# Kernel optimization log

Measured on AMD Instinct MI355X. Metric: run time of the kernel, lower is better.

Reference implementation:

```python
import jax, jax.numpy as jnp
import numpy as np

N_WORDS = 30000
EMB_DIM = 784  # 28*28
MAT_DIM = 28
BATCH = 1024
SEQ_LEN = 64


def setup_inputs() -> dict:
    key = jax.random.key(0)
    k_sent, k_tab = jax.random.split(key)
    # token ids in [0, n_words]; row 0 is the neutral (identity) / padding element
    sent = jax.random.randint(k_sent, (BATCH, SEQ_LEN), 0, N_WORDS + 1, dtype=jnp.int32).astype(jnp.int64)
    eye_flat = jnp.eye(MAT_DIM, dtype=jnp.float32).reshape(-1)
    # 'identity' init strategy: identity + small gaussian noise (scale kept small for stability of long products)
    table = eye_flat + 0.01 * jax.random.normal(k_tab, (N_WORDS + 1, EMB_DIM), dtype=jnp.float32)
    table = table.at[0].set(eye_flat)  # neutral element at padding_idx=0
    return {"sent": sent, "table": table}


def reference(sent, table):
    # sent: [B, S] int ids; table: [n_words+1, d*d]
    B, S = sent.shape
    d = MAT_DIM
    word_mats = table[sent].reshape(B, S, d, d)  # embedding lookup + unflatten
    # CMOW: continual multiplication cur = cur @ W_i, sequential over seq dim
    init = word_mats[:, 0]                      # [B, d, d]
    rest = jnp.moveaxis(word_mats[:, 1:], 1, 0)  # [S-1, B, d, d]

    def step(cur, w):
        return jnp.matmul(cur, w), None

    cur, _ = jax.lax.scan(step, init, rest)
    return cur.reshape(B, d * d)  # flatten matrix back to embedding
```

## Files before the change

kernel.cpp:

```cpp
#include <hip/hip_runtime.h>
#include <stdint.h>

#define SEQ 64
#define D 28
#define EMB 784
#define NW 4
#define CH 16
#define BUFF 832
#define CTW 36
#define CTSZ (32 * CTW)

typedef float float4v __attribute__((ext_vector_type(4)));
typedef __bf16 bf16x8 __attribute__((ext_vector_type(8)));

union FragU { unsigned u[4]; bf16x8 v; };

__device__ __forceinline__ unsigned fbits(float x) { union { float f; unsigned u; } t; t.f = x; return t.u; }
__device__ __forceinline__ float fof(unsigned u) { union { unsigned u; float f; } t; t.u = u; return t.f; }

__device__ __forceinline__ void split_frags(const float x[8], bf16x8& hi, bf16x8& lo)
{
    FragU H, L;
#pragma unroll
    for (int p = 0; p < 4; ++p) {
        unsigned ua = fbits(x[2 * p]), ub = fbits(x[2 * p + 1]);
        H.u[p] = (ua >> 16) | (ub & 0xFFFF0000u);
        unsigned la = fbits(x[2 * p]     - fof(ua & 0xFFFF0000u));
        unsigned lb = fbits(x[2 * p + 1] - fof(ub & 0xFFFF0000u));
        L.u[p] = (la >> 16) | (lb & 0xFFFF0000u);
    }
    hi = H.v; lo = L.v;
}

__device__ __forceinline__ void dma_row(const float* grow, float* lbuf, int lane)
{
    const char* g16 = (const char*)grow + lane * 16;
    const char* g4  = (const char*)grow + 3072 + lane * 4;
    char* l = (char*)lbuf;
    __builtin_amdgcn_global_load_lds((const __attribute__((address_space(1))) void*)(g16),
                                     (__attribute__((address_space(3))) void*)(l), 16, 0, 0);
    __builtin_amdgcn_global_load_lds((const __attribute__((address_space(1))) void*)(g16 + 1024),
                                     (__attribute__((address_space(3))) void*)(l + 1024), 16, 0, 0);
    __builtin_amdgcn_global_load_lds((const __attribute__((address_space(1))) void*)(g16 + 2048),
                                     (__attribute__((address_space(3))) void*)(l + 2048), 16, 0, 0);
    __builtin_amdgcn_global_load_lds((const __attribute__((address_space(1))) void*)(g4),
                                     (__attribute__((address_space(3))) void*)(l + 3072), 4, 0, 0);
}


__device__ __forceinline__ void publish_C(const float4v acc[2][2], float* dst, int lane)
{
    const int c = lane & 15;
    const int quad = lane >> 4;
#pragma unroll
    for (int R = 0; R < 2; ++R)
#pragma unroll
        for (int Cc = 0; Cc < 2; ++Cc)
#pragma unroll
            for (int i = 0; i < 4; ++i)
                dst[(16 * R + 4 * quad + i) * CTW + 16 * Cc + c] = acc[R][Cc][i];
}

__device__ __forceinline__ void load_A(const float* ct, int lane, bf16x8 Ah[2], bf16x8 Al[2])
{
    const int c = lane & 15;
    const int quad = lane >> 4;
    const bool q3 = (quad == 3);
#pragma unroll
    for (int R = 0; R < 2; ++R) {
        const float* ap = ct + (16 * R + c) * CTW + 8 * quad;
        float4v x0 = *(const float4v*)ap;
        float4v x1 = *(const float4v*)(ap + 4);
        if (q3) x1 = float4v{0.f, 0.f, 0.f, 0.f};
        float x[8] = {x0.x, x0.y, x0.z, x0.w, x1.x, x1.y, x1.z, x1.w};
        split_frags(x, Ah[R], Al[R]);
    }
}

__device__ __forceinline__ void load_B(const float* buf, int stride, int lane, bf16x8 Bh[2], bf16x8 Bl[2])
{
    const int c = lane & 15;
    const int quad = lane >> 4;
    const bool q3 = (quad == 3);
#pragma unroll
    for (int Cc = 0; Cc < 2; ++Cc) {
        const float* bp = buf + (8 * quad) * stride + 16 * Cc + c;
        float x[8];
#pragma unroll
        for (int t = 0; t < 8; ++t) x[t] = bp[t * stride];
        if (q3) { x[4] = 0.f; x[5] = 0.f; x[6] = 0.f; x[7] = 0.f; }
        split_frags(x, Bh[Cc], Bl[Cc]);
    }
}

__device__ __forceinline__ void mm_step(float4v acc[2][2], const bf16x8 Ah[2], const bf16x8 Al[2],
                                        const bf16x8 Bh[2], const bf16x8 Bl[2])
{
#pragma unroll
    for (int R = 0; R < 2; ++R)
#pragma unroll
        for (int Cc = 0; Cc < 2; ++Cc) {
            float4v d = {0.f, 0.f, 0.f, 0.f};
            d = __builtin_amdgcn_mfma_f32_16x16x32_bf16(Ah[R], Bh[Cc], d, 0, 0, 0);
            d = __builtin_amdgcn_mfma_f32_16x16x32_bf16(Ah[R], Bl[Cc], d, 0, 0, 0);
            d = __builtin_amdgcn_mfma_f32_16x16x32_bf16(Al[R], Bh[Cc], d, 0, 0, 0);
            acc[R][Cc] = d;
        }
}

template <int CNT, typename F>
__device__ __forceinline__ void mfma_chain(F rowptr,
                                           float* __restrict__ CTw,
                                           float* __restrict__ B0,
                                           float* __restrict__ B1,
                                           float4v acc[2][2],
                                           int lane)
{
    const int c = lane & 15;
    const int quad = lane >> 4;

    dma_row(rowptr(0), B0, lane);
    dma_row(rowptr(1), B1, lane);
    __builtin_amdgcn_s_waitcnt(0x0074);

#pragma unroll
    for (int R = 0; R < 2; ++R)
#pragma unroll
        for (int Cc = 0; Cc < 2; ++Cc)
#pragma unroll
            for (int i = 0; i < 4; ++i) {
                const int rr = 16 * R + 4 * quad + i;
                const int cc = 16 * Cc + c;
                acc[R][Cc][i] = B0[(rr < D ? rr : D - 1) * D + (cc < D ? cc : D - 1)];
            }
    __builtin_amdgcn_s_waitcnt(0xC07F);

#pragma unroll 1
    for (int j = 1; j < CNT; ++j) {
        const int jn = (j + 1 < CNT) ? (j + 1) : j;
        float* nB = (j & 1) ? B0 : B1;
        float* cB = (j & 1) ? B1 : B0;
        dma_row(rowptr(jn), nB, lane);

        publish_C(acc, CTw, lane);

        __builtin_amdgcn_sched_barrier(0);
        __builtin_amdgcn_s_waitcnt(0x0074);
        __builtin_amdgcn_sched_barrier(0);

        bf16x8 Ah[2], Al[2], Bh[2], Bl[2];
        load_A(CTw, lane, Ah, Al);
        load_B(cB, D, lane, Bh, Bl);
        mm_step(acc, Ah, Al, Bh, Bl);
    }
}

__device__ __forceinline__ void store_acc(const float4v acc[2][2],
                                          float* __restrict__ orow, int lane)
{
    const int c = lane & 15;
    const int quad = lane >> 4;
#pragma unroll
    for (int R = 0; R < 2; ++R)
#pragma unroll
        for (int Cc = 0; Cc < 2; ++Cc)
#pragma unroll
            for (int i = 0; i < 4; ++i) {
                const int row = 16 * R + 4 * quad + i;
                const int col = 16 * Cc + c;
                if (row < D && col < D) orow[row * D + col] = acc[R][Cc][i];
            }
}

__global__ __launch_bounds__(NW * 64, 1) void w2m_fused(
    const int* __restrict__ sent,
    const float* __restrict__ table,
    float* __restrict__ out)
{
    __shared__ float SH[NW * CTSZ + NW * 2 * BUFF] __attribute__((aligned(16)));
    const int lane = threadIdx.x & 63;
    const int wid  = threadIdx.x >> 6;
    const int b = blockIdx.x;

    float* CTw = &SH[wid * CTSZ];
    float* B0  = &SH[NW * CTSZ + wid * 2 * BUFF];
    float* B1  = B0 + BUFF;

    const int myidx = sent[b * SEQ + CH * wid + (lane & (CH - 1))];
    int jl[CH];
#pragma unroll
    for (int j = 0; j < CH; ++j) jl[j] = __builtin_amdgcn_readlane(myidx, j);

    float4v acc[2][2];
    mfma_chain<CH>([&](int j) { return table + (size_t)jl[j] * EMB; },
                   CTw, B0, B1, acc, lane);

    publish_C(acc, CTw, lane);
    __syncthreads();

    const int c = lane & 15;
    const int quad = lane >> 4;
#pragma unroll
    for (int R = 0; R < 2; ++R)
#pragma unroll
        for (int Cc = 0; Cc < 2; ++Cc)
#pragma unroll
            for (int i = 0; i < 4; ++i)
                acc[R][Cc][i] = SH[(16 * R + 4 * quad + i) * CTW + 16 * Cc + c];

    float* Sw = B0;
#pragma unroll 1
    for (int j = 1; j < NW; ++j) {
        publish_C(acc, Sw, lane);
        __builtin_amdgcn_sched_barrier(0);
        __builtin_amdgcn_s_waitcnt(0xC07F);
        __builtin_amdgcn_sched_barrier(0);
        bf16x8 Ah[2], Al[2], Bh[2], Bl[2];
        load_A(Sw, lane, Ah, Al);
        load_B(&SH[j * CTSZ], CTW, lane, Bh, Bl);
        mm_step(acc, Ah, Al, Bh, Bl);
    }

    if (wid == 0) store_acc(acc, out + (size_t)b * EMB, lane);
}

extern "C" void kernel_launch(void* const* d_in, const int* in_sizes, int n_in,
                              void* d_out, int out_size, void* d_ws, size_t ws_size,
                              hipStream_t stream) {
    const int* sent = (const int*)d_in[0];
    const float* table = (const float*)d_in[1];
    float* out = (float*)d_out;
    const int batch = in_sizes[0] / SEQ;
    (void)d_ws; (void)ws_size;

    hipLaunchKernelGGL(w2m_fused, dim3(batch), dim3(NW * 64), 0, stream,
                       sent, table, out);
}
```

Measured before the change: 157.3 us.

## Keep running product transposed in registers to skip LDS publish per step

The chain now computes the transposed product so the MFMA accumulator output can be fed directly back as the B operand, without writing C to LDS and re-reading it as A each step. Word matrices are read as the transposed A operand, and the cross-wave reduction reuses the DMA buffers as scratch. In exchange each step issues twice as many MFMAs (two half-K blocks with zero padding), and the reordered reduction order has to stay correct.

```diff
diff --git a/kernel.cpp b/kernel.cpp
--- a/kernel.cpp
+++ b/kernel.cpp
@@ -7,8 +7,7 @@
 #define NW 4
 #define CH 16
 #define BUFF 832
-#define CTW 36
-#define CTSZ (32 * CTW)
+#define SCRW 36
 
 typedef float float4v __attribute__((ext_vector_type(4)));
 typedef __bf16 bf16x8 __attribute__((ext_vector_type(8)));
@@ -30,6 +29,14 @@
         L.u[p] = (la >> 16) | (lb & 0xFFFF0000u);
     }
     hi = H.v; lo = L.v;
+}
+
+struct AB { bf16x8 h, l; };
+
+__device__ __forceinline__ AB make_frag4(const float y[4])
+{
+    float x[8] = { y[0], y[1], y[2], y[3], 0.f, 0.f, 0.f, 0.f };
+    AB r; split_frags(x, r.h, r.l); return r;
 }
 
 __device__ __forceinline__ void dma_row(const float* grow, float* lbuf, int lane)
@@ -47,74 +54,62 @@
                                      (__attribute__((address_space(3))) void*)(l + 3072), 4, 0, 0);
 }
 
-
-__device__ __forceinline__ void publish_C(const float4v acc[2][2], float* dst, int lane)
-{
-    const int c = lane & 15;
-    const int quad = lane >> 4;
-#pragma unroll
-    for (int R = 0; R < 2; ++R)
-#pragma unroll
-        for (int Cc = 0; Cc < 2; ++Cc)
-#pragma unroll
-            for (int i = 0; i < 4; ++i)
-                dst[(16 * R + 4 * quad + i) * CTW + 16 * Cc + c] = acc[R][Cc][i];
-}
-
-__device__ __forceinline__ void load_A(const float* ct, int lane, bf16x8 Ah[2], bf16x8 Al[2])
+__device__ __forceinline__ void stepT(const float* mat, int stride,
+                                      float4v acc[2][2], int lane)
 {
     const int c = lane & 15;
     const int quad = lane >> 4;
     const bool q3 = (quad == 3);
-#pragma unroll
-    for (int R = 0; R < 2; ++R) {
-        const float* ap = ct + (16 * R + c) * CTW + 8 * quad;
-        float4v x0 = *(const float4v*)ap;
-        float4v x1 = *(const float4v*)(ap + 4);
-        if (q3) x1 = float4v{0.f, 0.f, 0.f, 0.f};
-        float x[8] = {x0.x, x0.y, x0.z, x0.w, x1.x, x1.y, x1.z, x1.w};
-        split_frags(x, Ah[R], Al[R]);
-    }
-}
-
-__device__ __forceinline__ void load_B(const float* buf, int stride, int lane, bf16x8 Bh[2], bf16x8 Bl[2])
-{
-    const int c = lane & 15;
-    const int quad = lane >> 4;
-    const bool q3 = (quad == 3);
-#pragma unroll
-    for (int Cc = 0; Cc < 2; ++Cc) {
-        const float* bp = buf + (8 * quad) * stride + 16 * Cc + c;
-        float x[8];
-#pragma unroll
-        for (int t = 0; t < 8; ++t) x[t] = bp[t * stride];
-        if (q3) { x[4] = 0.f; x[5] = 0.f; x[6] = 0.f; x[7] = 0.f; }
-        split_frags(x, Bh[Cc], Bl[Cc]);
-    }
-}
-
-__device__ __forceinline__ void mm_step(float4v acc[2][2], const bf16x8 Ah[2], const bf16x8 Al[2],
-                                        const bf16x8 Bh[2], const bf16x8 Bl[2])
-{
-#pragma unroll
-    for (int R = 0; R < 2; ++R)
-#pragma unroll
-        for (int Cc = 0; Cc < 2; ++Cc) {
+
+    float av[2][2][4];
+#pragma unroll
+    for (int KB = 0; KB < 2; ++KB)
+#pragma unroll
+        for (int t = 0; t < 4; ++t) {
+            int k = 16 * KB + 4 * quad + t;
+            if (k > 27) k = 27;
+#pragma unroll
+            for (int Ro = 0; Ro < 2; ++Ro)
+                av[Ro][KB][t] = mat[k * stride + 16 * Ro + c];
+        }
+
+    AB Bf[2][2];
+#pragma unroll
+    for (int KB = 0; KB < 2; ++KB)
+#pragma unroll
+        for (int Co = 0; Co < 2; ++Co) {
+            float y[4] = { acc[KB][Co][0], acc[KB][Co][1], acc[KB][Co][2], acc[KB][Co][3] };
+            Bf[KB][Co] = make_frag4(y);
+        }
+
+    AB Af[2][2];
+#pragma unroll
+    for (int Ro = 0; Ro < 2; ++Ro)
+#pragma unroll
+        for (int KB = 0; KB < 2; ++KB) {
+            float y[4] = { av[Ro][KB][0], av[Ro][KB][1], av[Ro][KB][2], av[Ro][KB][3] };
+            if (q3 && KB == 1) { y[0] = y[1] = y[2] = y[3] = 0.f; }
+            Af[Ro][KB] = make_frag4(y);
+        }
+
+#pragma unroll
+    for (int Ro = 0; Ro < 2; ++Ro)
+#pragma unroll
+        for (int Co = 0; Co < 2; ++Co) {
             float4v d = {0.f, 0.f, 0.f, 0.f};
-            d = __builtin_amdgcn_mfma_f32_16x16x32_bf16(Ah[R], Bh[Cc], d, 0, 0, 0);
-            d = __builtin_amdgcn_mfma_f32_16x16x32_bf16(Ah[R], Bl[Cc], d, 0, 0, 0);
-            d = __builtin_amdgcn_mfma_f32_16x16x32_bf16(Al[R], Bh[Cc], d, 0, 0, 0);
-            acc[R][Cc] = d;
+#pragma unroll
+            for (int KB = 0; KB < 2; ++KB) {
+                d = __builtin_amdgcn_mfma_f32_16x16x32_bf16(Af[Ro][KB].h, Bf[KB][Co].h, d, 0, 0, 0);
+                d = __builtin_amdgcn_mfma_f32_16x16x32_bf16(Af[Ro][KB].h, Bf[KB][Co].l, d, 0, 0, 0);
+                d = __builtin_amdgcn_mfma_f32_16x16x32_bf16(Af[Ro][KB].l, Bf[KB][Co].h, d, 0, 0, 0);
+            }
+            acc[Ro][Co] = d;
         }
 }
 
 template <int CNT, typename F>
-__device__ __forceinline__ void mfma_chain(F rowptr,
-                                           float* __restrict__ CTw,
-                                           float* __restrict__ B0,
-                                           float* __restrict__ B1,
-                                           float4v acc[2][2],
-                                           int lane)
+__device__ __forceinline__ void chainT(F rowptr, float* B0, float* B1,
+                                       float4v acc[2][2], int lane)
 {
     const int c = lane & 15;
     const int quad = lane >> 4;
@@ -126,13 +121,10 @@
 #pragma unroll
     for (int R = 0; R < 2; ++R)
 #pragma unroll
-        for (int Cc = 0; Cc < 2; ++Cc)
-#pragma unroll
-            for (int i = 0; i < 4; ++i) {
-                const int rr = 16 * R + 4 * quad + i;
-                const int cc = 16 * Cc + c;
-                acc[R][Cc][i] = B0[(rr < D ? rr : D - 1) * D + (cc < D ? cc : D - 1)];
-            }
+        for (int Cc = 0; Cc < 2; ++Cc) {
+            int rcl = 16 * Cc + c; if (rcl > 27) rcl = 27;
+            acc[R][Cc] = *(const float4v*)&B0[rcl * D + 16 * R + 4 * quad];
+        }
     __builtin_amdgcn_s_waitcnt(0xC07F);
 
 #pragma unroll 1
@@ -142,49 +134,26 @@
         float* cB = (j & 1) ? B1 : B0;
         dma_row(rowptr(jn), nB, lane);
 
-        publish_C(acc, CTw, lane);
-
         __builtin_amdgcn_sched_barrier(0);
         __builtin_amdgcn_s_waitcnt(0x0074);
         __builtin_amdgcn_sched_barrier(0);
 
-        bf16x8 Ah[2], Al[2], Bh[2], Bl[2];
-        load_A(CTw, lane, Ah, Al);
-        load_B(cB, D, lane, Bh, Bl);
-        mm_step(acc, Ah, Al, Bh, Bl);
+        stepT(cB, D, acc, lane);
     }
 }
 
-__device__ __forceinline__ void store_acc(const float4v acc[2][2],
-                                          float* __restrict__ orow, int lane)
-{
-    const int c = lane & 15;
-    const int quad = lane >> 4;
-#pragma unroll
-    for (int R = 0; R < 2; ++R)
-#pragma unroll
-        for (int Cc = 0; Cc < 2; ++Cc)
-#pragma unroll
-            for (int i = 0; i < 4; ++i) {
-                const int row = 16 * R + 4 * quad + i;
-                const int col = 16 * Cc + c;
-                if (row < D && col < D) orow[row * D + col] = acc[R][Cc][i];
-            }
-}
-
-__global__ __launch_bounds__(NW * 64, 1) void w2m_fused(
+__global__ __launch_bounds__(NW * 64, 1) void w2m_fusedT(
     const int* __restrict__ sent,
     const float* __restrict__ table,
     float* __restrict__ out)
 {
-    __shared__ float SH[NW * CTSZ + NW * 2 * BUFF] __attribute__((aligned(16)));
+    __shared__ float SH[NW * 2 * BUFF] __attribute__((aligned(16)));
     const int lane = threadIdx.x & 63;
     const int wid  = threadIdx.x >> 6;
     const int b = blockIdx.x;
 
-    float* CTw = &SH[wid * CTSZ];
-    float* B0  = &SH[NW * CTSZ + wid * 2 * BUFF];
-    float* B1  = B0 + BUFF;
+    float* B0 = &SH[wid * 2 * BUFF];
+    float* B1 = B0 + BUFF;
 
     const int myidx = sent[b * SEQ + CH * wid + (lane & (CH - 1))];
     int jl[CH];
@@ -192,36 +161,48 @@
     for (int j = 0; j < CH; ++j) jl[j] = __builtin_amdgcn_readlane(myidx, j);
 
     float4v acc[2][2];
-    mfma_chain<CH>([&](int j) { return table + (size_t)jl[j] * EMB; },
-                   CTw, B0, B1, acc, lane);
-
-    publish_C(acc, CTw, lane);
-    __syncthreads();
+    chainT<CH>([&](int j) { return table + (size_t)jl[j] * EMB; },
+               B0, B1, acc, lane);
 
     const int c = lane & 15;
     const int quad = lane >> 4;
+
+    __builtin_amdgcn_s_waitcnt(0x0070);
+    __builtin_amdgcn_sched_barrier(0);
+    float* SCR = &SH[wid * 2 * BUFF];
 #pragma unroll
     for (int R = 0; R < 2; ++R)
 #pragma unroll
         for (int Cc = 0; Cc < 2; ++Cc)
 #pragma unroll
             for (int i = 0; i < 4; ++i)
-                acc[R][Cc][i] = SH[(16 * R + 4 * quad + i) * CTW + 16 * Cc + c];
-
-    float* Sw = B0;
+                SCR[(16 * R + 4 * quad + i) * SCRW + 16 * Cc + c] = acc[R][Cc][i];
+    __syncthreads();
+
+    const float* S3 = &SH[3 * 2 * BUFF];
+#pragma unroll
+    for (int R = 0; R < 2; ++R)
+#pragma unroll
+        for (int Cc = 0; Cc < 2; ++Cc)
+            acc[R][Cc] = *(const float4v*)&S3[(16 * Cc + c) * SCRW + 16 * R + 4 * quad];
+
 #pragma unroll 1
-    for (int j = 1; j < NW; ++j) {
-        publish_C(acc, Sw, lane);
-        __builtin_amdgcn_sched_barrier(0);
-        __builtin_amdgcn_s_waitcnt(0xC07F);
-        __builtin_amdgcn_sched_barrier(0);
-        bf16x8 Ah[2], Al[2], Bh[2], Bl[2];
-        load_A(Sw, lane, Ah, Al);
-        load_B(&SH[j * CTSZ], CTW, lane, Bh, Bl);
-        mm_step(acc, Ah, Al, Bh, Bl);
+    for (int j = 2; j >= 0; --j)
+        stepT(&SH[j * 2 * BUFF], SCRW, acc, lane);
+
+    if (wid == 0) {
+        float* orow = out + (size_t)b * EMB;
+#pragma unroll
+        for (int R = 0; R < 2; ++R)
+#pragma unroll
+            for (int Cc = 0; Cc < 2; ++Cc)
+#pragma unroll
+                for (int i = 0; i < 4; ++i) {
+                    const int row = 16 * R + 4 * quad + i;
+                    const int col = 16 * Cc + c;
+                    if (row < D && col < D) orow[row * D + col] = acc[R][Cc][i];
+                }
     }
-
-    if (wid == 0) store_acc(acc, out + (size_t)b * EMB, lane);
 }
 
 extern "C" void kernel_launch(void* const* d_in, const int* in_sizes, int n_in,
@@ -233,6 +214,6 @@
     const int batch = in_sizes[0] / SEQ;
     (void)d_ws; (void)ws_size;
 
-    hipLaunchKernelGGL(w2m_fused, dim3(batch), dim3(NW * 64), 0, stream,
+    hipLaunchKernelGGL(w2m_fusedT, dim3(batch), dim3(NW * 64), 0, stream,
                        sent, table, out);
 }
```

Measured after the change: 159.8 us. No clear change (+1.6%).
